# Kernel optimization log

Hardware: AMD Instinct MI355X
Metric: run time of the kernel (lower is better)

The kernel has to match this reference:

```python
import jax, jax.numpy as jnp
import numpy as np

N_NODES = 100000
SAMPLES = 16


def setup_inputs() -> dict:
    key = jax.random.key(0)
    ks = jax.random.split(key, 9)
    x = jax.random.normal(ks[0], (N_NODES, 128), dtype=jnp.float32)
    neigh_idx = jax.random.randint(ks[1], (N_NODES, SAMPLES), 0, N_NODES)
    batch = jax.random.randint(ks[2], (8192,), 0, N_NODES)
    W1 = jax.random.normal(ks[3], (256, 128), dtype=jnp.float32) * 0.05
    b1 = jax.random.normal(ks[4], (128,), dtype=jnp.float32) * 0.05
    W2 = jax.random.normal(ks[5], (256, 128), dtype=jnp.float32) * 0.05
    b2 = jax.random.normal(ks[6], (128,), dtype=jnp.float32) * 0.05
    Wout = jax.random.normal(ks[7], (128, 64), dtype=jnp.float32) * 0.05
    bout = jax.random.normal(ks[8], (64,), dtype=jnp.float32) * 0.05
    return {"x": x, "neigh_idx": neigh_idx, "batch": batch,
            "W1": W1, "b1": b1, "W2": W2, "b2": b2,
            "Wout": Wout, "bout": bout}


def _sage_layer(h, neigh_idx, W, b):
    # h: [N, d]; gather sampled neighbors -> [N, S, d]; max-aggregate; concat-linear
    neigh = h[neigh_idx]                     # irregular gather, memory-bound core
    agg = jnp.max(neigh, axis=1)             # MaxAggregation over samples
    feats = jnp.concatenate([h, agg], axis=-1)  # [N, 2d]
    return feats @ W + b


def reference(x, neigh_idx, batch, W1, b1, W2, b2, Wout, bout):
    # layer 1: relu(Linear(concat(x, max_neigh(x))))
    h1 = jax.nn.relu(_sage_layer(x, neigh_idx, W1, b1))
    # layer 2 (== n_layers): Linear output (no relu) fed straight into proj_out
    h2 = _sage_layer(h1, neigh_idx, W2, b2)
    out = h2 @ Wout + bout                   # proj_out (Dropout is eval identity)
    return out[batch]
```

## Files before the change

kernel.cpp:

```cpp
#include <hip/hip_runtime.h>
#include <cmath>
#include <cstdint>

#define N_NODES 100000
#define SAMPLES 16
#define DIM 128
#define NBATCH 8192

#define H2STR 132

typedef _Float16 half8 __attribute__((ext_vector_type(8)));
typedef float floatx4 __attribute__((ext_vector_type(4)));

__device__ __forceinline__ half8 h8max(half8 a, half8 b) {
    half8 r;
#pragma unroll
    for (int i = 0; i < 8; ++i) r[i] = (a[i] > b[i]) ? a[i] : b[i];
    return r;
}

__global__ __launch_bounds__(256) void setup_kernel(
    const float* __restrict__ x,
    const float* __restrict__ W1,
    const float* __restrict__ W2,
    int* __restrict__ flags,
    _Float16* __restrict__ xh,
    _Float16* __restrict__ W1sw,
    _Float16* __restrict__ W2sw) {
    const int bid = blockIdx.x;
    if (bid < 6250) {
        const size_t base = ((size_t)bid * 256 + threadIdx.x) * 8;
        const float4* xp = (const float4*)(x + base);
        const float4 a = xp[0], b = xp[1];
        half8 v;
        v[0] = (_Float16)a.x; v[1] = (_Float16)a.y;
        v[2] = (_Float16)a.z; v[3] = (_Float16)a.w;
        v[4] = (_Float16)b.x; v[5] = (_Float16)b.y;
        v[6] = (_Float16)b.z; v[7] = (_Float16)b.w;
        *(half8*)(xh + base) = v;
    } else if (bid < 6641) {
        const int i = (bid - 6250) * 256 + threadIdx.x;
        if (i < N_NODES) flags[i] = 0;
    } else {
        const int tid = (bid - 6641) * 256 + threadIdx.x;
        const int which = tid >> 12;
        const int r = tid & 4095;
        const int kb = r >> 9, nb = (r >> 6) & 7, lane = r & 63;
        const int q = lane >> 4, c = lane & 15;
        const float* W = which ? W2 : W1;
        _Float16* O = which ? W2sw : W1sw;
        const int k0 = kb * 32 + q * 8;
        const int n = nb * 16 + c;
        half8 v;
#pragma unroll
        for (int j = 0; j < 8; ++j) v[j] = (_Float16)W[(size_t)(k0 + j) * DIM + n];
        *(half8*)(O + (size_t)r * 8) = v;
    }
}

__global__ __launch_bounds__(256) void mark_flags(const int* __restrict__ batch,
                                                  const int* __restrict__ nidx,
                                                  int* __restrict__ flags) {
    int j = blockIdx.x * blockDim.x + threadIdx.x;
    if (j >= NBATCH) return;
    int b = batch[j];
    flags[b] = 1;
    const int* row = nidx + (size_t)b * SAMPLES;
#pragma unroll
    for (int s = 0; s < SAMPLES; ++s) flags[row[s]] = 1;
}

__global__ __launch_bounds__(256) void layer1_kernel(
    const _Float16* __restrict__ xh,
    const int* __restrict__ nidx,
    const _Float16* __restrict__ W1sw,
    const float* __restrict__ b1,
    const int* __restrict__ flags,
    _Float16* __restrict__ h1h) {
    const int wave = threadIdx.x >> 6;
    const int lane = threadIdx.x & 63;
    const int q = lane >> 4;
    const int c = lane & 15;
    const int w0 = blockIdx.x * 64 + wave * 16;

    const int i = w0 + c;
    const bool fi = (i < N_NODES) && flags[i];

    half8 sk[4], mk[4];
#pragma unroll
    for (int j = 0; j < 4; ++j) {
#pragma unroll
        for (int e = 0; e < 8; ++e) { sk[j][e] = (_Float16)0.f; mk[j][e] = (_Float16)(-60000.f); }
    }

    if (fi) {
        const _Float16* rp = xh + (size_t)i * DIM + q * 8;
#pragma unroll
        for (int j = 0; j < 4; ++j) sk[j] = *(const half8*)(rp + j * 32);

        const int4* ip = (const int4*)(nidx + (size_t)i * SAMPLES);
        const int4 i0 = ip[0], i1 = ip[1], i2 = ip[2], i3 = ip[3];
        const int idx[16] = {i0.x, i0.y, i0.z, i0.w, i1.x, i1.y, i1.z, i1.w,
                             i2.x, i2.y, i2.z, i2.w, i3.x, i3.y, i3.z, i3.w};
#pragma unroll
        for (int s = 0; s < SAMPLES; s += 2) {
            const _Float16* ra = xh + (size_t)idx[s] * DIM + q * 8;
            const _Float16* rb = xh + (size_t)idx[s + 1] * DIM + q * 8;
            half8 va[4], vb[4];
#pragma unroll
            for (int j = 0; j < 4; ++j) va[j] = *(const half8*)(ra + j * 32);
#pragma unroll
            for (int j = 0; j < 4; ++j) vb[j] = *(const half8*)(rb + j * 32);
#pragma unroll
            for (int j = 0; j < 4; ++j) mk[j] = h8max(mk[j], h8max(va[j], vb[j]));
        }
    }

    floatx4 acc[8];
#pragma unroll
    for (int nb = 0; nb < 8; ++nb) acc[nb] = (floatx4){0.f, 0.f, 0.f, 0.f};
#pragma unroll
    for (int kb = 0; kb < 8; ++kb) {
        const half8 a = (kb < 4) ? sk[kb] : mk[kb - 4];
#pragma unroll
        for (int nb = 0; nb < 8; ++nb) {
            const half8 b = *(const half8*)(W1sw + (size_t)((kb * 8 + nb) * 64 + lane) * 8);
            acc[nb] = __builtin_amdgcn_mfma_f32_16x16x32_f16(a, b, acc[nb], 0, 0, 0);
        }
    }

#pragma unroll
    for (int r = 0; r < 4; ++r) {
        const int node = w0 + q * 4 + r;
        if (node >= N_NODES || !flags[node]) continue;
#pragma unroll
        for (int nb = 0; nb < 8; ++nb) {
            const int n = nb * 16 + c;
            const float v = fmaxf(acc[nb][r] + b1[n], 0.f);
            h1h[(size_t)node * DIM + n] = (_Float16)v;
        }
    }
}

__global__ __launch_bounds__(64) void layer2_kernel(
    const _Float16* __restrict__ h1h,
    const int* __restrict__ nidx,
    const int* __restrict__ batch,
    const _Float16* __restrict__ W2sw,
    const float* __restrict__ b2,
    const float* __restrict__ Wout,
    const float* __restrict__ bout,
    float* __restrict__ out) {
    const int lane = threadIdx.x;
    const int q = lane >> 4, c = lane & 15;
    const int w0 = blockIdx.x * 16;

    __shared__ __align__(16) float h2s[16 * H2STR];

    const int node = batch[w0 + c];
    half8 sk[4], mk[4];
    {
        const _Float16* rp = h1h + (size_t)node * DIM + q * 8;
#pragma unroll
        for (int j = 0; j < 4; ++j) sk[j] = *(const half8*)(rp + j * 32);
#pragma unroll
        for (int j = 0; j < 4; ++j)
#pragma unroll
            for (int e = 0; e < 8; ++e) mk[j][e] = (_Float16)(-60000.f);
        const int4* ip = (const int4*)(nidx + (size_t)node * SAMPLES);
        const int4 i0 = ip[0], i1 = ip[1], i2 = ip[2], i3 = ip[3];
        const int idx[16] = {i0.x, i0.y, i0.z, i0.w, i1.x, i1.y, i1.z, i1.w,
                             i2.x, i2.y, i2.z, i2.w, i3.x, i3.y, i3.z, i3.w};
#pragma unroll
        for (int s = 0; s < SAMPLES; s += 2) {
            const _Float16* ra = h1h + (size_t)idx[s] * DIM + q * 8;
            const _Float16* rb = h1h + (size_t)idx[s + 1] * DIM + q * 8;
            half8 va[4], vb[4];
#pragma unroll
            for (int j = 0; j < 4; ++j) va[j] = *(const half8*)(ra + j * 32);
#pragma unroll
            for (int j = 0; j < 4; ++j) vb[j] = *(const half8*)(rb + j * 32);
#pragma unroll
            for (int j = 0; j < 4; ++j) mk[j] = h8max(mk[j], h8max(va[j], vb[j]));
        }
    }

    floatx4 acc[8];
#pragma unroll
    for (int nb = 0; nb < 8; ++nb) acc[nb] = (floatx4){0.f, 0.f, 0.f, 0.f};
#pragma unroll
    for (int kb = 0; kb < 8; ++kb) {
        const half8 a = (kb < 4) ? sk[kb] : mk[kb - 4];
#pragma unroll
        for (int nb = 0; nb < 8; ++nb) {
            const half8 b = *(const half8*)(W2sw + (size_t)((kb * 8 + nb) * 64 + lane) * 8);
            acc[nb] = __builtin_amdgcn_mfma_f32_16x16x32_f16(a, b, acc[nb], 0, 0, 0);
        }
    }

#pragma unroll
    for (int nb = 0; nb < 8; ++nb) {
        const int n = nb * 16 + c;
        const float bias = b2[n];
#pragma unroll
        for (int r = 0; r < 4; ++r)
            h2s[(q * 4 + r) * H2STR + n] = acc[nb][r] + bias;
    }

    float accs[16];
    const float bo = bout[lane];
#pragma unroll
    for (int m = 0; m < 16; ++m) accs[m] = bo;
    for (int k4 = 0; k4 < DIM; k4 += 4) {
        float wv[4];
#pragma unroll
        for (int j = 0; j < 4; ++j) wv[j] = Wout[(size_t)(k4 + j) * 64 + lane];
#pragma unroll
        for (int m = 0; m < 16; ++m) {
            const float4 f = *(const float4*)&h2s[m * H2STR + k4];
            accs[m] += f.x * wv[0] + f.y * wv[1] + f.z * wv[2] + f.w * wv[3];
        }
    }
#pragma unroll
    for (int m = 0; m < 16; ++m)
        out[(size_t)(w0 + m) * 64 + lane] = accs[m];
}

extern "C" void kernel_launch(void* const* d_in, const int* in_sizes, int n_in,
                              void* d_out, int out_size, void* d_ws, size_t ws_size,
                              hipStream_t stream) {
    const float* x    = (const float*)d_in[0];
    const int* nidx   = (const int*)d_in[1];
    const int* batch  = (const int*)d_in[2];
    const float* W1   = (const float*)d_in[3];
    const float* b1   = (const float*)d_in[4];
    const float* W2   = (const float*)d_in[5];
    const float* b2   = (const float*)d_in[6];
    const float* Wout = (const float*)d_in[7];
    const float* bout = (const float*)d_in[8];
    float* out        = (float*)d_out;

    int* flags      = (int*)d_ws;
    _Float16* W1sw  = (_Float16*)((char*)d_ws + 409600);
    _Float16* W2sw  = (_Float16*)((char*)d_ws + 475136);
    _Float16* xh    = (_Float16*)((char*)d_ws + 540672);
    _Float16* h1h   = (_Float16*)((char*)d_ws + 26140672);

    setup_kernel<<<6673, 256, 0, stream>>>(x, W1, W2, flags, xh, W1sw, W2sw);
    mark_flags<<<32, 256, 0, stream>>>(batch, nidx, flags);
    layer1_kernel<<<(N_NODES + 63) / 64, 256, 0, stream>>>(xh, nidx, W1sw, b1, flags, h1h);
    layer2_kernel<<<NBATCH / 16, 64, 0, stream>>>(h1h, nidx, batch, W2sw, b2, Wout, bout, out);
}
```

Before: 204.4 us.

## Fuse flag marking into setup, deepen gathers, spread layer2 over four waves

Removes the per-call zeroing of the flags buffer and folds the flag-marking pass into the setup kernel, saving one launch and a 400 KB memset. Layer 1 now issues all 16 neighbor loads per column chunk at once and reduces them as a tree, with 32-bit byte offsets, to raise memory-level parallelism; launch bounds request 3 blocks per SIMD. Layer 2 moves from one 64-thread wave per 16 nodes to 256 threads: the gather goes through shared memory, and the MFMA and output projection are split across waves. Because flags are never cleared and the check is `== 1`, leftover or garbage values only cause extra nodes to be computed, so results stay correct.

```diff
diff --git a/kernel.cpp b/kernel.cpp
--- a/kernel.cpp
+++ b/kernel.cpp
@@ -7,6 +7,7 @@
 #define DIM 128
 #define NBATCH 8192
 
+#define FSTR 264
 #define H2STR 132
 
 typedef _Float16 half8 __attribute__((ext_vector_type(8)));
@@ -23,6 +24,8 @@
     const float* __restrict__ x,
     const float* __restrict__ W1,
     const float* __restrict__ W2,
+    const int* __restrict__ batch,
+    const int* __restrict__ nidx,
     int* __restrict__ flags,
     _Float16* __restrict__ xh,
     _Float16* __restrict__ W1sw,
@@ -38,11 +41,8 @@
         v[4] = (_Float16)b.x; v[5] = (_Float16)b.y;
         v[6] = (_Float16)b.z; v[7] = (_Float16)b.w;
         *(half8*)(xh + base) = v;
-    } else if (bid < 6641) {
-        const int i = (bid - 6250) * 256 + threadIdx.x;
-        if (i < N_NODES) flags[i] = 0;
-    } else {
-        const int tid = (bid - 6641) * 256 + threadIdx.x;
+    } else if (bid < 6282) {
+        const int tid = (bid - 6250) * 256 + threadIdx.x;
         const int which = tid >> 12;
         const int r = tid & 4095;
         const int kb = r >> 9, nb = (r >> 6) & 7, lane = r & 63;
@@ -55,22 +55,19 @@
 #pragma unroll
         for (int j = 0; j < 8; ++j) v[j] = (_Float16)W[(size_t)(k0 + j) * DIM + n];
         *(half8*)(O + (size_t)r * 8) = v;
-    }
-}
-
-__global__ __launch_bounds__(256) void mark_flags(const int* __restrict__ batch,
-                                                  const int* __restrict__ nidx,
-                                                  int* __restrict__ flags) {
-    int j = blockIdx.x * blockDim.x + threadIdx.x;
-    if (j >= NBATCH) return;
-    int b = batch[j];
-    flags[b] = 1;
-    const int* row = nidx + (size_t)b * SAMPLES;
-#pragma unroll
-    for (int s = 0; s < SAMPLES; ++s) flags[row[s]] = 1;
-}
-
-__global__ __launch_bounds__(256) void layer1_kernel(
+    } else {
+        const int j = (bid - 6282) * 256 + threadIdx.x;
+        if (j < NBATCH) {
+            const int b = batch[j];
+            flags[b] = 1;
+            const int* row = nidx + (size_t)b * SAMPLES;
+#pragma unroll
+            for (int s = 0; s < SAMPLES; ++s) flags[row[s]] = 1;
+        }
+    }
+}
+
+__global__ __launch_bounds__(256, 3) void layer1_kernel(
     const _Float16* __restrict__ xh,
     const int* __restrict__ nidx,
     const _Float16* __restrict__ W1sw,
@@ -84,35 +81,41 @@
     const int w0 = blockIdx.x * 64 + wave * 16;
 
     const int i = w0 + c;
-    const bool fi = (i < N_NODES) && flags[i];
+    const bool fi = (i < N_NODES) && (flags[i] == 1);
 
     half8 sk[4], mk[4];
 #pragma unroll
-    for (int j = 0; j < 4; ++j) {
+    for (int j = 0; j < 4; ++j)
 #pragma unroll
         for (int e = 0; e < 8; ++e) { sk[j][e] = (_Float16)0.f; mk[j][e] = (_Float16)(-60000.f); }
-    }
 
     if (fi) {
-        const _Float16* rp = xh + (size_t)i * DIM + q * 8;
-#pragma unroll
-        for (int j = 0; j < 4; ++j) sk[j] = *(const half8*)(rp + j * 32);
-
+        const char* xb = (const char*)xh;
         const int4* ip = (const int4*)(nidx + (size_t)i * SAMPLES);
         const int4 i0 = ip[0], i1 = ip[1], i2 = ip[2], i3 = ip[3];
-        const int idx[16] = {i0.x, i0.y, i0.z, i0.w, i1.x, i1.y, i1.z, i1.w,
-                             i2.x, i2.y, i2.z, i2.w, i3.x, i3.y, i3.z, i3.w};
-#pragma unroll
-        for (int s = 0; s < SAMPLES; s += 2) {
-            const _Float16* ra = xh + (size_t)idx[s] * DIM + q * 8;
-            const _Float16* rb = xh + (size_t)idx[s + 1] * DIM + q * 8;
-            half8 va[4], vb[4];
-#pragma unroll
-            for (int j = 0; j < 4; ++j) va[j] = *(const half8*)(ra + j * 32);
-#pragma unroll
-            for (int j = 0; j < 4; ++j) vb[j] = *(const half8*)(rb + j * 32);
-#pragma unroll
-            for (int j = 0; j < 4; ++j) mk[j] = h8max(mk[j], h8max(va[j], vb[j]));
+        const int qb = q * 16;
+        const int soff = i * 256 + qb;
+        int off[16];
+        off[0]  = i0.x * 256 + qb; off[1]  = i0.y * 256 + qb;
+        off[2]  = i0.z * 256 + qb; off[3]  = i0.w * 256 + qb;
+        off[4]  = i1.x * 256 + qb; off[5]  = i1.y * 256 + qb;
+        off[6]  = i1.z * 256 + qb; off[7]  = i1.w * 256 + qb;
+        off[8]  = i2.x * 256 + qb; off[9]  = i2.y * 256 + qb;
+        off[10] = i2.z * 256 + qb; off[11] = i2.w * 256 + qb;
+        off[12] = i3.x * 256 + qb; off[13] = i3.y * 256 + qb;
+        off[14] = i3.z * 256 + qb; off[15] = i3.w * 256 + qb;
+#pragma unroll
+        for (int j = 0; j < 4; ++j) {
+            sk[j] = *(const half8*)(xb + soff + j * 64);
+            half8 v[16];
+#pragma unroll
+            for (int s = 0; s < 16; ++s)
+                v[s] = *(const half8*)(xb + off[s] + j * 64);
+#pragma unroll
+            for (int s = 0; s < 8; ++s) v[s] = h8max(v[s], v[s + 8]);
+#pragma unroll
+            for (int s = 0; s < 4; ++s) v[s] = h8max(v[s], v[s + 4]);
+            mk[j] = h8max(h8max(v[0], v[1]), h8max(v[2], v[3]));
         }
     }
 
@@ -132,7 +135,7 @@
 #pragma unroll
     for (int r = 0; r < 4; ++r) {
         const int node = w0 + q * 4 + r;
-        if (node >= N_NODES || !flags[node]) continue;
+        if (node >= N_NODES || flags[node] != 1) continue;
 #pragma unroll
         for (int nb = 0; nb < 8; ++nb) {
             const int n = nb * 16 + c;
@@ -142,7 +145,7 @@
     }
 }
 
-__global__ __launch_bounds__(64) void layer2_kernel(
+__global__ __launch_bounds__(256) void layer2_kernel(
     const _Float16* __restrict__ h1h,
     const int* __restrict__ nidx,
     const int* __restrict__ batch,
@@ -151,79 +154,86 @@
     const float* __restrict__ Wout,
     const float* __restrict__ bout,
     float* __restrict__ out) {
-    const int lane = threadIdx.x;
+    const int t = threadIdx.x;
+    const int wave = t >> 6;
+    const int lane = t & 63;
     const int q = lane >> 4, c = lane & 15;
     const int w0 = blockIdx.x * 16;
 
+    __shared__ __align__(16) _Float16 feats[16 * FSTR];
     __shared__ __align__(16) float h2s[16 * H2STR];
 
-    const int node = batch[w0 + c];
-    half8 sk[4], mk[4];
     {
-        const _Float16* rp = h1h + (size_t)node * DIM + q * 8;
-#pragma unroll
-        for (int j = 0; j < 4; ++j) sk[j] = *(const half8*)(rp + j * 32);
-#pragma unroll
-        for (int j = 0; j < 4; ++j)
-#pragma unroll
-            for (int e = 0; e < 8; ++e) mk[j][e] = (_Float16)(-60000.f);
+        const int m = t >> 4;
+        const int cl = t & 15;
+        const int node = batch[w0 + m];
+        const char* hb = (const char*)h1h;
+        const int cb = cl * 16;
+        const half8 self = *(const half8*)(hb + node * 256 + cb);
         const int4* ip = (const int4*)(nidx + (size_t)node * SAMPLES);
         const int4 i0 = ip[0], i1 = ip[1], i2 = ip[2], i3 = ip[3];
-        const int idx[16] = {i0.x, i0.y, i0.z, i0.w, i1.x, i1.y, i1.z, i1.w,
-                             i2.x, i2.y, i2.z, i2.w, i3.x, i3.y, i3.z, i3.w};
-#pragma unroll
-        for (int s = 0; s < SAMPLES; s += 2) {
-            const _Float16* ra = h1h + (size_t)idx[s] * DIM + q * 8;
-            const _Float16* rb = h1h + (size_t)idx[s + 1] * DIM + q * 8;
-            half8 va[4], vb[4];
-#pragma unroll
-            for (int j = 0; j < 4; ++j) va[j] = *(const half8*)(ra + j * 32);
-#pragma unroll
-            for (int j = 0; j < 4; ++j) vb[j] = *(const half8*)(rb + j * 32);
-#pragma unroll
-            for (int j = 0; j < 4; ++j) mk[j] = h8max(mk[j], h8max(va[j], vb[j]));
-        }
-    }
-
-    floatx4 acc[8];
-#pragma unroll
-    for (int nb = 0; nb < 8; ++nb) acc[nb] = (floatx4){0.f, 0.f, 0.f, 0.f};
+        int off[16];
+        off[0]  = i0.x * 256 + cb; off[1]  = i0.y * 256 + cb;
+        off[2]  = i0.z * 256 + cb; off[3]  = i0.w * 256 + cb;
+        off[4]  = i1.x * 256 + cb; off[5]  = i1.y * 256 + cb;
+        off[6]  = i1.z * 256 + cb; off[7]  = i1.w * 256 + cb;
+        off[8]  = i2.x * 256 + cb; off[9]  = i2.y * 256 + cb;
+        off[10] = i2.z * 256 + cb; off[11] = i2.w * 256 + cb;
+        off[12] = i3.x * 256 + cb; off[13] = i3.y * 256 + cb;
+        off[14] = i3.z * 256 + cb; off[15] = i3.w * 256 + cb;
+        half8 v[16];
+#pragma unroll
+        for (int s = 0; s < 16; ++s) v[s] = *(const half8*)(hb + off[s]);
+#pragma unroll
+        for (int s = 0; s < 8; ++s) v[s] = h8max(v[s], v[s + 8]);
+#pragma unroll
+        for (int s = 0; s < 4; ++s) v[s] = h8max(v[s], v[s + 4]);
+        const half8 mx = h8max(h8max(v[0], v[1]), h8max(v[2], v[3]));
+        *(half8*)(feats + m * FSTR + cl * 8) = self;
+        *(half8*)(feats + m * FSTR + DIM + cl * 8) = mx;
+    }
+    __syncthreads();
+
+    const int nb0 = wave * 2;
+    floatx4 acc[2];
+    acc[0] = (floatx4){0.f, 0.f, 0.f, 0.f};
+    acc[1] = (floatx4){0.f, 0.f, 0.f, 0.f};
 #pragma unroll
     for (int kb = 0; kb < 8; ++kb) {
-        const half8 a = (kb < 4) ? sk[kb] : mk[kb - 4];
-#pragma unroll
-        for (int nb = 0; nb < 8; ++nb) {
-            const half8 b = *(const half8*)(W2sw + (size_t)((kb * 8 + nb) * 64 + lane) * 8);
-            acc[nb] = __builtin_amdgcn_mfma_f32_16x16x32_f16(a, b, acc[nb], 0, 0, 0);
-        }
-    }
-
-#pragma unroll
-    for (int nb = 0; nb < 8; ++nb) {
-        const int n = nb * 16 + c;
+        const half8 a = *(const half8*)(feats + c * FSTR + kb * 32 + q * 8);
+#pragma unroll
+        for (int j = 0; j < 2; ++j) {
+            const half8 b = *(const half8*)(W2sw + (size_t)((kb * 8 + nb0 + j) * 64 + lane) * 8);
+            acc[j] = __builtin_amdgcn_mfma_f32_16x16x32_f16(a, b, acc[j], 0, 0, 0);
+        }
+    }
+#pragma unroll
+    for (int j = 0; j < 2; ++j) {
+        const int n = (nb0 + j) * 16 + c;
         const float bias = b2[n];
 #pragma unroll
         for (int r = 0; r < 4; ++r)
-            h2s[(q * 4 + r) * H2STR + n] = acc[nb][r] + bias;
-    }
-
-    float accs[16];
+            h2s[(q * 4 + r) * H2STR + n] = acc[j][r] + bias;
+    }
+    __syncthreads();
+
+    float accs[4];
     const float bo = bout[lane];
 #pragma unroll
-    for (int m = 0; m < 16; ++m) accs[m] = bo;
+    for (int r = 0; r < 4; ++r) accs[r] = bo;
     for (int k4 = 0; k4 < DIM; k4 += 4) {
         float wv[4];
 #pragma unroll
         for (int j = 0; j < 4; ++j) wv[j] = Wout[(size_t)(k4 + j) * 64 + lane];
 #pragma unroll
-        for (int m = 0; m < 16; ++m) {
-            const float4 f = *(const float4*)&h2s[m * H2STR + k4];
-            accs[m] += f.x * wv[0] + f.y * wv[1] + f.z * wv[2] + f.w * wv[3];
-        }
-    }
-#pragma unroll
-    for (int m = 0; m < 16; ++m)
-        out[(size_t)(w0 + m) * 64 + lane] = accs[m];
+        for (int r = 0; r < 4; ++r) {
+            const float4 f = *(const float4*)&h2s[(wave * 4 + r) * H2STR + k4];
+            accs[r] += f.x * wv[0] + f.y * wv[1] + f.z * wv[2] + f.w * wv[3];
+        }
+    }
+#pragma unroll
+    for (int r = 0; r < 4; ++r)
+        out[(size_t)(w0 + wave * 4 + r) * 64 + lane] = accs[r];
 }
 
 extern "C" void kernel_launch(void* const* d_in, const int* in_sizes, int n_in,
@@ -246,8 +256,7 @@
     _Float16* xh    = (_Float16*)((char*)d_ws + 540672);
     _Float16* h1h   = (_Float16*)((char*)d_ws + 26140672);
 
-    setup_kernel<<<6673, 256, 0, stream>>>(x, W1, W2, flags, xh, W1sw, W2sw);
-    mark_flags<<<32, 256, 0, stream>>>(batch, nidx, flags);
+    setup_kernel<<<6314, 256, 0, stream>>>(x, W1, W2, batch, nidx, flags, xh, W1sw, W2sw);
     layer1_kernel<<<(N_NODES + 63) / 64, 256, 0, stream>>>(xh, nidx, W1sw, b1, flags, h1h);
-    layer2_kernel<<<NBATCH / 16, 64, 0, stream>>>(h1h, nidx, batch, W2sw, b2, Wout, bout, out);
-}
+    layer2_kernel<<<NBATCH / 16, 256, 0, stream>>>(h1h, nidx, batch, W2sw, b2, Wout, bout, out);
+}
```

Result: faster. 193.3 us (-5.4%).
